# Kernel optimization log

Measured on AMD Instinct MI355X. Metric: run time of the kernel, lower is better.

The kernel has to match this reference:

```python
import jax, jax.numpy as jnp
import numpy as np

WS = 49        # window size
NH = 8         # num heads


def setup_inputs() -> dict:
    key = jax.random.key(0)
    k1, k2, k3 = jax.random.split(key, 3)
    B, N, C = 4, 50176, 512
    x = jax.random.normal(k1, (B, N, C), dtype=jnp.float32)
    w_qkv = jax.random.normal(k2, (3 * C, C), dtype=jnp.float32) * (C ** -0.5)
    b_qkv = jnp.zeros((3 * C,), dtype=jnp.float32)
    w_proj = jax.random.normal(k3, (C, C), dtype=jnp.float32) * (C ** -0.5)
    b_proj = jnp.zeros((C,), dtype=jnp.float32)
    return {"x": x, "w_qkv": w_qkv, "b_qkv": b_qkv, "w_proj": w_proj, "b_proj": b_proj}


def reference(x, w_qkv, b_qkv, w_proj, b_proj):
    B, N, C = x.shape
    w = N // WS
    hd = C // NH
    scale = hd ** -0.5
    # shuffle: 'b (ws w) c -> (b w) ws c'  (outer factor is ws -> strided windows)
    xw = x.reshape(B, WS, w, C).transpose(0, 2, 1, 3).reshape(B * w, WS, C)
    qkv = xw @ w_qkv.T + b_qkv                       # [(B w), WS, 3C]
    qkv = qkv.reshape(B * w, WS, 3, NH, hd)
    q = qkv[:, :, 0].transpose(0, 2, 1, 3) * scale   # [(B w), NH, WS, hd]
    k = qkv[:, :, 1].transpose(0, 2, 1, 3)
    v = qkv[:, :, 2].transpose(0, 2, 1, 3)
    attn = jax.nn.softmax(jnp.einsum('bhqd,bhkd->bhqk', q, k), axis=-1)
    out = jnp.einsum('bhqk,bhkd->bhqd', attn, v)     # [(B w), NH, WS, hd]
    out = out.transpose(0, 2, 1, 3).reshape(B * w, WS, C)
    out = out @ w_proj.T + b_proj
    # unshuffle: '(b w) ws c -> b (ws w) c'
    out = out.reshape(B, w, WS, C).transpose(0, 2, 1, 3).reshape(B, N, C)
    return out
```

## Files before the change

kernel.cpp:

```cpp
#include <hip/hip_runtime.h>
#include <cstdint>
#include <cstddef>


typedef __bf16 bf16x8 __attribute__((ext_vector_type(8)));
typedef __bf16 bf16x4 __attribute__((ext_vector_type(4)));
typedef float  f32x4  __attribute__((ext_vector_type(4)));

#define MFMA_BF16(a, b, c) __builtin_amdgcn_mfma_f32_16x16x32_bf16((a), (b), (c), 0, 0, 0)

static __device__ __forceinline__ int swzi(int row, int col) {
  return col ^ ((row & 7) << 3);
}
static __device__ __forceinline__ int gswz(int row, int col) {
  return col ^ (((row >> 1) & 3) << 3);
}

typedef __attribute__((address_space(1))) const void gconst_t;
typedef __attribute__((address_space(3))) void lds_t;
static __device__ __forceinline__ void gload16(const void* g, void* l) {
  __builtin_amdgcn_global_load_lds((gconst_t*)g, (lds_t*)l, 16, 0, 0);
}

__global__ void prep_weights(const float* __restrict__ wqkv,
                             const float* __restrict__ bqkv,
                             const float* __restrict__ wproj,
                             __bf16* __restrict__ wqkv_bf,
                             __bf16* __restrict__ wproj_bf,
                             float* __restrict__ bq_s) {
  const int stride = gridDim.x * blockDim.x;
  const int t0 = blockIdx.x * blockDim.x + threadIdx.x;
  for (int i = t0; i < 1536 * 512; i += stride) {
    float v = wqkv[i];
    if (i < 512 * 512) v *= 0.125f;
    wqkv_bf[i] = (__bf16)v;
  }
  for (int i = t0; i < 512 * 512; i += stride) wproj_bf[i] = (__bf16)wproj[i];
  for (int i = t0; i < 1536; i += stride)      bq_s[i] = (i < 512 ? 0.125f : 1.0f) * bqkv[i];
}

__global__ void prep_x(const float* __restrict__ x, __bf16* __restrict__ xb) {
  const size_t total  = (size_t)200704 * 512 / 8;
  const size_t stride = (size_t)gridDim.x * blockDim.x;
  for (size_t i = (size_t)blockIdx.x * blockDim.x + threadIdx.x; i < total; i += stride) {
    const float4 a = *(const float4*)(x + i * 8);
    const float4 b = *(const float4*)(x + i * 8 + 4);
    bf16x8 t;
    t[0] = (__bf16)a.x; t[1] = (__bf16)a.y; t[2] = (__bf16)a.z; t[3] = (__bf16)a.w;
    t[4] = (__bf16)b.x; t[5] = (__bf16)b.y; t[6] = (__bf16)b.z; t[7] = (__bf16)b.w;
    *(bf16x8*)(xb + i * 8) = t;
  }
}

template<bool OUT_F32>
__launch_bounds__(256)
__global__ void gemm_bt(const __bf16* __restrict__ Ab,
                        const __bf16* __restrict__ Bw,
                        const float* __restrict__ bias,
                        void* __restrict__ Cv,
                        int Mtiles, int Ntiles) {
  __shared__ __align__(16) __bf16 sA[2][128 * 32];
  __shared__ __align__(16) __bf16 sB[2][128 * 32];

  const int tid  = threadIdx.x;
  const int lane = tid & 63;
  const int l15  = lane & 15;
  const int kg   = ((lane >> 4) & 3) * 8;
  const int r4   = ((lane >> 4) & 3) * 4;
  const int wv   = tid >> 6, wm = wv >> 1, wn = wv & 1;

  const int nwg = Mtiles * Ntiles;
  const int cpx = nwg >> 3;
  const int wg  = (blockIdx.x & 7) * cpx + (blockIdx.x >> 3);
  const int mt  = wg / Ntiles;
  const int nt  = wg % Ntiles;
  const size_t m0 = (size_t)mt * 128;
  const int    n0 = nt * 128;

  const int srow  = tid >> 2;
  const int scol8 = ((tid & 3) * 8) ^ (((tid >> 3) & 3) << 3);

  f32x4 acc[4][4];
  const f32x4 zf = {0.f, 0.f, 0.f, 0.f};
#pragma unroll
  for (int i = 0; i < 4; ++i)
#pragma unroll
    for (int j = 0; j < 4; ++j) acc[i][j] = zf;

#pragma unroll
  for (int j = 0; j < 2; ++j) {
    gload16(Bw + ((size_t)(n0 + j * 64 + srow)) * 512 + scol8,
            &sB[0][0] + (size_t)tid * 8 + j * 2048);
    gload16(Ab + (m0 + j * 64 + srow) * 512 + scol8,
            &sA[0][0] + (size_t)tid * 8 + j * 2048);
  }
  __syncthreads();

  int buf = 0;
  for (int kt = 0; kt < 16; ++kt) {
    const int k1 = (kt + 1) * 32;
    if (kt < 15) {
#pragma unroll
      for (int j = 0; j < 2; ++j) {
        gload16(Bw + ((size_t)(n0 + j * 64 + srow)) * 512 + k1 + scol8,
                &sB[buf ^ 1][0] + (size_t)tid * 8 + j * 2048);
        gload16(Ab + (m0 + j * 64 + srow) * 512 + k1 + scol8,
                &sA[buf ^ 1][0] + (size_t)tid * 8 + j * 2048);
      }
    }
    bf16x8 af[4], bfr[4];
#pragma unroll
    for (int m = 0; m < 4; ++m) {
      const int row = wm * 64 + m * 16 + l15;
      af[m] = *(const bf16x8*)&sA[buf][row * 32 + gswz(row, kg)];
    }
#pragma unroll
    for (int n = 0; n < 4; ++n) {
      const int row = wn * 64 + n * 16 + l15;
      bfr[n] = *(const bf16x8*)&sB[buf][row * 32 + gswz(row, kg)];
    }
#pragma unroll
    for (int m = 0; m < 4; ++m)
#pragma unroll
      for (int n = 0; n < 4; ++n)
        acc[m][n] = MFMA_BF16(af[m], bfr[n], acc[m][n]);

    __syncthreads();
    buf ^= 1;
  }

  const int Nld = Ntiles * 128;
#pragma unroll
  for (int n = 0; n < 4; ++n) {
    const int col = n0 + wn * 64 + n * 16 + l15;
    const float bb = bias[col];
#pragma unroll
    for (int m = 0; m < 4; ++m) {
#pragma unroll
      for (int r = 0; r < 4; ++r) {
        const size_t row = m0 + wm * 64 + m * 16 + r4 + r;
        const float v = acc[m][n][r] + bb;
        if (OUT_F32) ((float*)Cv)[row * (size_t)Nld + col] = v;
        else         ((__bf16*)Cv)[row * (size_t)Nld + col] = (__bf16)v;
      }
    }
  }
}

__launch_bounds__(512)
__global__ void attn_win(const __bf16* __restrict__ qkv, __bf16* __restrict__ O) {
  __shared__ __align__(16) __bf16 vT[8 * 64 * 64];
  __shared__ __align__(16) __bf16 sP[8][16 * 64];

  const int tid  = threadIdx.x;
  const int lane = tid & 63;
  const int h    = tid >> 6;
  const int l15  = lane & 15;
  const int kg   = ((lane >> 4) & 3) * 8;
  const int r4   = ((lane >> 4) & 3) * 4;

  const int blk = blockIdx.x;
  const int b   = blk >> 10;
  const int wi  = blk & 1023;
  const size_t tokbase = (size_t)b * 50176 + wi;

  const int MOFF[4] = {0, 16, 32, 33};
  const float NEG_INF = -__builtin_inff();

  bf16x8 aq[4][2], bk[4][2];
#pragma unroll
  for (int mt = 0; mt < 4; ++mt) {
    const size_t tok = tokbase + (size_t)(MOFF[mt] + l15) * 1024;
#pragma unroll
    for (int ks = 0; ks < 2; ++ks) {
      aq[mt][ks] = *(const bf16x8*)(qkv + tok * 1536 +       h * 64 + ks * 32 + kg);
      bk[mt][ks] = *(const bf16x8*)(qkv + tok * 1536 + 512 + h * 64 + ks * 32 + kg);
    }
  }

  for (int i = tid; i < 8 * 64 * 16; i += 512) {
    const int k = 48 + (i & 15);
    if (k != 48) {
      const int n  = (i >> 4) & 63;
      const int hh = i >> 10;
      vT[hh * 4096 + n * 64 + (k ^ ((n & 7) << 3))] = (__bf16)0.0f;
    }
  }
  for (int i = tid; i < 49 * 64; i += 512) {
    const int s  = i >> 6;
    const int c8 = (i & 63) * 8;
    bf16x8 v8 = *(const bf16x8*)(qkv + (tokbase + (size_t)s * 1024) * 1536 + 1024 + c8);
    const int hh = c8 >> 6;
#pragma unroll
    for (int j = 0; j < 8; ++j) {
      const int n = (c8 & 63) + j;
      vT[hh * 4096 + n * 64 + (s ^ ((n & 7) << 3))] = v8[j];
    }
  }
  __syncthreads();

  bf16x8 bv[4][2];
#pragma unroll
  for (int ntv = 0; ntv < 4; ++ntv) {
    const int n = ntv * 16 + l15;
#pragma unroll
    for (int ks = 0; ks < 2; ++ks)
      bv[ntv][ks] = *(const bf16x8*)&vT[h * 4096 + n * 64 + ((ks * 32 + kg) ^ ((n & 7) << 3))];
  }

  f32x4 accS[4][4];
  const f32x4 zf = {0.f, 0.f, 0.f, 0.f};
#pragma unroll
  for (int m = 0; m < 4; ++m)
#pragma unroll
    for (int n = 0; n < 4; ++n) accS[m][n] = zf;
#pragma unroll
  for (int ks = 0; ks < 2; ++ks)
#pragma unroll
    for (int m = 0; m < 4; ++m)
#pragma unroll
      for (int n = 0; n < 4; ++n)
        accS[m][n] = MFMA_BF16(aq[m][ks], bk[n][ks], accS[m][n]);

#pragma unroll
  for (int mt = 0; mt < 4; ++mt) {
#pragma unroll
    for (int r = 0; r < 4; ++r) {
      const int prow = r4 + r;
      const float sv0 = accS[mt][0][r];
      const float sv1 = accS[mt][1][r];
      const float sv2 = accS[mt][2][r];
      const float sv3 = (l15 == 15) ? accS[mt][3][r] : NEG_INF;
      float mx = fmaxf(fmaxf(sv0, sv1), fmaxf(sv2, sv3));
      mx = fmaxf(mx, __shfl_xor(mx, 1));
      mx = fmaxf(mx, __shfl_xor(mx, 2));
      mx = fmaxf(mx, __shfl_xor(mx, 4));
      mx = fmaxf(mx, __shfl_xor(mx, 8));
      const float e0 = __expf(sv0 - mx);
      const float e1 = __expf(sv1 - mx);
      const float e2 = __expf(sv2 - mx);
      const float e3 = __expf(sv3 - mx);
      float sum = e0 + e1 + e2 + e3;
      sum += __shfl_xor(sum, 1);
      sum += __shfl_xor(sum, 2);
      sum += __shfl_xor(sum, 4);
      sum += __shfl_xor(sum, 8);
      const float inv = 1.0f / sum;
      sP[h][prow * 64 + swzi(prow, 0  + l15)] = (__bf16)(e0 * inv);
      sP[h][prow * 64 + swzi(prow, 16 + l15)] = (__bf16)(e1 * inv);
      sP[h][prow * 64 + swzi(prow, 32 + l15)] = (__bf16)(e2 * inv);
      if (l15 == 15) sP[h][prow * 64 + swzi(prow, 48)] = (__bf16)(e3 * inv);
      if (l15 < 15)  sP[h][prow * 64 + swzi(prow, 49 + l15)] = (__bf16)0.0f;
    }
    bf16x8 ap[2];
#pragma unroll
    for (int ks = 0; ks < 2; ++ks)
      ap[ks] = *(const bf16x8*)&sP[h][l15 * 64 + swzi(l15, ks * 32 + kg)];
    f32x4 accO[4];
#pragma unroll
    for (int n = 0; n < 4; ++n) accO[n] = zf;
#pragma unroll
    for (int ks = 0; ks < 2; ++ks)
#pragma unroll
      for (int n = 0; n < 4; ++n)
        accO[n] = MFMA_BF16(ap[ks], bv[n][ks], accO[n]);
#pragma unroll
    for (int n = 0; n < 4; ++n) {
#pragma unroll
      for (int r = 0; r < 4; ++r) {
        const int row = MOFF[mt] + r4 + r;
        O[(tokbase + (size_t)row * 1024) * 512 + h * 64 + n * 16 + l15] =
            (__bf16)accO[n][r];
      }
    }
  }
}

__launch_bounds__(256, 2)
__global__ void swin_attn_fused(const float* __restrict__ x,
                                const __bf16* __restrict__ wqkv_bf,
                                const float* __restrict__ bq_s,
                                const __bf16* __restrict__ wproj_bf,
                                const float* __restrict__ bproj,
                                float* __restrict__ out) {
  __shared__ __align__(16) __bf16 s_xw[49 * 512];
  __shared__ __align__(16) __bf16 s_q [49 * 64];
  __shared__ __align__(16) __bf16 s_k [49 * 64];
  __shared__ __align__(16) __bf16 s_vT[64 * 64];
  __shared__ __align__(16) __bf16 s_p [49 * 64];

  const int tid  = threadIdx.x;
  const int lane = tid & 63;
  const int wv   = tid >> 6;
  const int l15  = lane & 15;
  const int kg   = (lane >> 4) * 8;
  const int r4   = (lane >> 4) * 4;
  const int blk = blockIdx.x;
  const int b   = blk >> 10;
  const int wi  = blk & 1023;
  const int MOFF[4] = {0, 16, 32, 33};
  const float NEG_INF = -__builtin_inff();

  for (int i = tid; i < 64 * 64; i += 256) s_vT[i] = (__bf16)0.0f;
  const float* xwin = x + ((size_t)b * 50176 + (size_t)wi) * 512;
  for (int idx = tid; idx < 49 * 128; idx += 256) {
    const int row = idx >> 7;
    const int c4  = (idx & 127) * 4;
    const float4 v = *(const float4*)(xwin + (size_t)row * (1024 * 512) + c4);
    bf16x4 t;
    t.x = (__bf16)v.x; t.y = (__bf16)v.y; t.z = (__bf16)v.z; t.w = (__bf16)v.w;
    *(bf16x4*)&s_xw[row * 512 + swzi(row, c4)] = t;
  }
  f32x4 accF[4][8];
  const f32x4 zf = {0.f, 0.f, 0.f, 0.f};
#pragma unroll
  for (int m = 0; m < 4; ++m)
#pragma unroll
    for (int n = 0; n < 8; ++n) accF[m][n] = zf;
  __syncthreads();

  for (int h = 0; h < 8; ++h) {
    f32x4 accA[4][3];
#pragma unroll
    for (int m = 0; m < 4; ++m)
#pragma unroll
      for (int n = 0; n < 3; ++n) accA[m][n] = zf;
    const __bf16* pB[3];
    float biasv[3];
#pragma unroll
    for (int nt = 0; nt < 3; ++nt) {
      const int c  = wv * 48 + nt * 16 + l15;
      const int wr = (c < 64) ? (h * 64 + c)
                   : (c < 128) ? (512 + h * 64 + (c - 64))
                               : (1024 + h * 64 + (c - 128));
      pB[nt]    = wqkv_bf + (size_t)wr * 512 + kg;
      biasv[nt] = bq_s[wr];
    }
#pragma unroll
    for (int ks = 0; ks < 16; ++ks) {
      bf16x8 a[4], bb[3];
#pragma unroll
      for (int mt = 0; mt < 4; ++mt) {
        const int row = MOFF[mt] + l15;
        a[mt] = *(const bf16x8*)&s_xw[row * 512 + swzi(row, ks * 32 + kg)];
      }
#pragma unroll
      for (int nt = 0; nt < 3; ++nt) bb[nt] = *(const bf16x8*)(pB[nt] + ks * 32);
#pragma unroll
      for (int mt = 0; mt < 4; ++mt)
#pragma unroll
        for (int nt = 0; nt < 3; ++nt)
          accA[mt][nt] = MFMA_BF16(a[mt], bb[nt], accA[mt][nt]);
    }
#pragma unroll
    for (int nt = 0; nt < 3; ++nt) {
      const int c = wv * 48 + nt * 16 + l15;
#pragma unroll
      for (int mt = 0; mt < 4; ++mt) {
#pragma unroll
        for (int r = 0; r < 4; ++r) {
          const int row = MOFF[mt] + r4 + r;
          const __bf16 bvv = (__bf16)(accA[mt][nt][r] + biasv[nt]);
          if (c < 64)       s_q[row * 64 + swzi(row, c)] = bvv;
          else if (c < 128) s_k[row * 64 + swzi(row, c - 64)] = bvv;
          else {
            const int vr = c - 128;
            s_vT[vr * 64 + swzi(vr, row)] = bvv;
          }
        }
      }
    }
    __syncthreads();

    const int R = MOFF[wv];
    bf16x8 aq[2], bkf[4][2];
#pragma unroll
    for (int ks2 = 0; ks2 < 2; ++ks2) {
      const int row = R + l15;
      aq[ks2] = *(const bf16x8*)&s_q[row * 64 + swzi(row, ks2 * 32 + kg)];
    }
#pragma unroll
    for (int nt = 0; nt < 4; ++nt) {
      const int row = MOFF[nt] + l15;
#pragma unroll
      for (int ks2 = 0; ks2 < 2; ++ks2)
        bkf[nt][ks2] = *(const bf16x8*)&s_k[row * 64 + swzi(row, ks2 * 32 + kg)];
    }
    f32x4 accS[4];
#pragma unroll
    for (int n = 0; n < 4; ++n) accS[n] = zf;
#pragma unroll
    for (int ks2 = 0; ks2 < 2; ++ks2)
#pragma unroll
      for (int nt = 0; nt < 4; ++nt)
        accS[nt] = MFMA_BF16(aq[ks2], bkf[nt][ks2], accS[nt]);
#pragma unroll
    for (int r = 0; r < 4; ++r) {
      const int row = R + r4 + r;
      const float sv0 = accS[0][r];
      const float sv1 = accS[1][r];
      const float sv2 = accS[2][r];
      const float sv3 = (l15 == 15) ? accS[3][r] : NEG_INF;
      float m = fmaxf(fmaxf(sv0, sv1), fmaxf(sv2, sv3));
      m = fmaxf(m, __shfl_xor(m, 1));
      m = fmaxf(m, __shfl_xor(m, 2));
      m = fmaxf(m, __shfl_xor(m, 4));
      m = fmaxf(m, __shfl_xor(m, 8));
      const float e0 = __expf(sv0 - m);
      const float e1 = __expf(sv1 - m);
      const float e2 = __expf(sv2 - m);
      const float e3 = __expf(sv3 - m);
      float s = e0 + e1 + e2 + e3;
      s += __shfl_xor(s, 1);
      s += __shfl_xor(s, 2);
      s += __shfl_xor(s, 4);
      s += __shfl_xor(s, 8);
      const float inv = 1.0f / s;
      s_p[row * 64 + swzi(row, 0  + l15)] = (__bf16)(e0 * inv);
      s_p[row * 64 + swzi(row, 16 + l15)] = (__bf16)(e1 * inv);
      s_p[row * 64 + swzi(row, 32 + l15)] = (__bf16)(e2 * inv);
      if (l15 == 15) s_p[row * 64 + swzi(row, 48)] = (__bf16)(e3 * inv);
      if (l15 < 15)  s_p[row * 64 + swzi(row, 49 + l15)] = (__bf16)0.0f;
    }
    bf16x8 ap[2], bv2[4][2];
#pragma unroll
    for (int ks2 = 0; ks2 < 2; ++ks2) {
      const int row = R + l15;
      ap[ks2] = *(const bf16x8*)&s_p[row * 64 + swzi(row, ks2 * 32 + kg)];
    }
#pragma unroll
    for (int nt = 0; nt < 4; ++nt) {
      const int row = nt * 16 + l15;
#pragma unroll
      for (int ks2 = 0; ks2 < 2; ++ks2)
        bv2[nt][ks2] = *(const bf16x8*)&s_vT[row * 64 + swzi(row, ks2 * 32 + kg)];
    }
    __syncthreads();
    f32x4 accO[4];
#pragma unroll
    for (int n = 0; n < 4; ++n) accO[n] = zf;
#pragma unroll
    for (int ks2 = 0; ks2 < 2; ++ks2)
#pragma unroll
      for (int nt = 0; nt < 4; ++nt)
        accO[nt] = MFMA_BF16(ap[ks2], bv2[nt][ks2], accO[nt]);
#pragma unroll
    for (int nt = 0; nt < 4; ++nt) {
#pragma unroll
      for (int r = 0; r < 4; ++r) {
        const int row = R + r4 + r;
        s_p[row * 64 + swzi(row, nt * 16 + l15)] = (__bf16)accO[nt][r];
      }
    }
    __syncthreads();
#pragma unroll
    for (int ks2 = 0; ks2 < 2; ++ks2) {
      bf16x8 ao[4], bw[8];
#pragma unroll
      for (int mt = 0; mt < 4; ++mt) {
        const int row = MOFF[mt] + l15;
        ao[mt] = *(const bf16x8*)&s_p[row * 64 + swzi(row, ks2 * 32 + kg)];
      }
#pragma unroll
      for (int nt = 0; nt < 8; ++nt) {
        const int cc = wv * 128 + nt * 16 + l15;
        bw[nt] = *(const bf16x8*)(wproj_bf + (size_t)cc * 512 + h * 64 + ks2 * 32 + kg);
      }
#pragma unroll
      for (int mt = 0; mt < 4; ++mt)
#pragma unroll
        for (int nt = 0; nt < 8; ++nt)
          accF[mt][nt] = MFMA_BF16(ao[mt], bw[nt], accF[mt][nt]);
    }
  }
#pragma unroll
  for (int nt = 0; nt < 8; ++nt) {
    const int cc = wv * 128 + nt * 16 + l15;
    const float bp = bproj[cc];
#pragma unroll
    for (int mt = 0; mt < 4; ++mt) {
#pragma unroll
      for (int r = 0; r < 4; ++r) {
        const int row = MOFF[mt] + r4 + r;
        if (mt < 3 || (r4 + r) == 15) {
          out[((size_t)b * 50176 + (size_t)row * 1024 + (size_t)wi) * 512 + cc] =
              accF[mt][nt][r] + bp;
        }
      }
    }
  }
}

extern "C" void kernel_launch(void* const* d_in, const int* in_sizes, int n_in,
                              void* d_out, int out_size, void* d_ws, size_t ws_size,
                              hipStream_t stream) {
  const float* x      = (const float*)d_in[0];
  const float* w_qkv  = (const float*)d_in[1];
  const float* b_qkv  = (const float*)d_in[2];
  const float* w_proj = (const float*)d_in[3];
  const float* b_proj = (const float*)d_in[4];
  float* outp = (float*)d_out;

  const size_t QKV_E = (size_t)200704 * 1536;
  const size_t O_E   = (size_t)200704 * 512;
  const size_t NEED  = (QKV_E + O_E + 786432 + 262144) * 2 + 1536 * 4;

  if (ws_size >= NEED) {
    __bf16* qkv      = (__bf16*)d_ws;
    __bf16* Obuf     = qkv + QKV_E;
    __bf16* wqkv_bf  = Obuf + O_E;
    __bf16* wproj_bf = wqkv_bf + 786432;
    float*  bq_s     = (float*)(wproj_bf + 262144);

    prep_weights<<<512, 256, 0, stream>>>(w_qkv, b_qkv, w_proj, wqkv_bf, wproj_bf, bq_s);
    prep_x<<<2048, 256, 0, stream>>>(x, Obuf);
    gemm_bt<false><<<1568 * 12, 256, 0, stream>>>(Obuf, wqkv_bf, bq_s, qkv, 1568, 12);
    attn_win<<<4096, 512, 0, stream>>>(qkv, Obuf);
    gemm_bt<true ><<<1568 * 4,  256, 0, stream>>>(Obuf, wproj_bf, b_proj, outp, 1568, 4);
  } else {
    __bf16* wqkv_bf  = (__bf16*)d_ws;
    __bf16* wproj_bf = wqkv_bf + 1536 * 512;
    float*  bq_s     = (float*)(wproj_bf + 512 * 512);
    prep_weights<<<1024, 256, 0, stream>>>(w_qkv, b_qkv, w_proj, wqkv_bf, wproj_bf, bq_s);
    swin_attn_fused<<<4096, 256, 0, stream>>>(x, wqkv_bf, bq_s, wproj_bf, b_proj, outp);
  }
}
```

Measured before the change: 1.156 ms.

## Replace 128x128 GEMM with 256x256 tile, 512-thread kernel using raw barriers

Both projection GEMMs move from 128x128x32 tiles with 256 threads to 256x256x64 tiles with 512 threads and 8 waves. Each wave now computes a 128x64 sub-tile. The LDS staging uses an XOR chunk swizzle and double buffering with explicit vmcnt waits and raw s_barrier in place of __syncthreads, and MFMA priority is raised via s_setprio. The aim is more data reuse per byte loaded and less synchronisation overhead. In exchange, LDS use is 128KB per block, giving one block per CU, and register pressure is higher.

```diff
diff --git a/kernel.cpp b/kernel.cpp
--- a/kernel.cpp
+++ b/kernel.cpp
@@ -11,9 +11,6 @@
 
 static __device__ __forceinline__ int swzi(int row, int col) {
   return col ^ ((row & 7) << 3);
-}
-static __device__ __forceinline__ int gswz(int row, int col) {
-  return col ^ (((row >> 1) & 3) << 3);
 }
 
 typedef __attribute__((address_space(1))) const void gconst_t;
@@ -21,6 +18,9 @@
 static __device__ __forceinline__ void gload16(const void* g, void* l) {
   __builtin_amdgcn_global_load_lds((gconst_t*)g, (lds_t*)l, 16, 0, 0);
 }
+
+#define RAW_BAR()  asm volatile("s_barrier" ::: "memory")
+#define WAITV(N)   asm volatile("s_waitcnt vmcnt(" #N ")" ::: "memory")
 
 __global__ void prep_weights(const float* __restrict__ wqkv,
                              const float* __restrict__ bqkv,
@@ -53,92 +53,110 @@
 }
 
 template<bool OUT_F32>
-__launch_bounds__(256)
-__global__ void gemm_bt(const __bf16* __restrict__ Ab,
+__launch_bounds__(512, 1)
+__global__ void gemm256(const __bf16* __restrict__ Ab,
                         const __bf16* __restrict__ Bw,
                         const float* __restrict__ bias,
                         void* __restrict__ Cv,
                         int Mtiles, int Ntiles) {
-  __shared__ __align__(16) __bf16 sA[2][128 * 32];
-  __shared__ __align__(16) __bf16 sB[2][128 * 32];
+  __shared__ __align__(16) __bf16 sA[2][256 * 64];
+  __shared__ __align__(16) __bf16 sB[2][256 * 64];
 
   const int tid  = threadIdx.x;
   const int lane = tid & 63;
   const int l15  = lane & 15;
-  const int kg   = ((lane >> 4) & 3) * 8;
-  const int r4   = ((lane >> 4) & 3) * 4;
-  const int wv   = tid >> 6, wm = wv >> 1, wn = wv & 1;
+  const int kgc  = (lane >> 4) & 3;
+  const int r4   = kgc * 4;
+  const int wv   = tid >> 6;
+  const int wm   = wv >> 2, wn = wv & 3;
 
   const int nwg = Mtiles * Ntiles;
   const int cpx = nwg >> 3;
   const int wg  = (blockIdx.x & 7) * cpx + (blockIdx.x >> 3);
   const int mt  = wg / Ntiles;
   const int nt  = wg % Ntiles;
-  const size_t m0 = (size_t)mt * 128;
-  const int    n0 = nt * 128;
-
-  const int srow  = tid >> 2;
-  const int scol8 = ((tid & 3) * 8) ^ (((tid >> 3) & 3) << 3);
-
-  f32x4 acc[4][4];
+  const size_t m0 = (size_t)mt * 256;
+  const int    n0 = nt * 256;
+
+  const int srow   = tid >> 3;
+  const int schunk = (tid & 7) ^ (srow & 7);
+
+  f32x4 acc[8][4];
   const f32x4 zf = {0.f, 0.f, 0.f, 0.f};
 #pragma unroll
-  for (int i = 0; i < 4; ++i)
+  for (int i = 0; i < 8; ++i)
 #pragma unroll
     for (int j = 0; j < 4; ++j) acc[i][j] = zf;
 
-#pragma unroll
-  for (int j = 0; j < 2; ++j) {
-    gload16(Bw + ((size_t)(n0 + j * 64 + srow)) * 512 + scol8,
-            &sB[0][0] + (size_t)tid * 8 + j * 2048);
-    gload16(Ab + (m0 + j * 64 + srow) * 512 + scol8,
-            &sA[0][0] + (size_t)tid * 8 + j * 2048);
-  }
-  __syncthreads();
-
-  int buf = 0;
-  for (int kt = 0; kt < 16; ++kt) {
-    const int k1 = (kt + 1) * 32;
-    if (kt < 15) {
-#pragma unroll
-      for (int j = 0; j < 2; ++j) {
-        gload16(Bw + ((size_t)(n0 + j * 64 + srow)) * 512 + k1 + scol8,
-                &sB[buf ^ 1][0] + (size_t)tid * 8 + j * 2048);
-        gload16(Ab + (m0 + j * 64 + srow) * 512 + k1 + scol8,
-                &sA[buf ^ 1][0] + (size_t)tid * 8 + j * 2048);
-      }
-    }
-    bf16x8 af[4], bfr[4];
-#pragma unroll
-    for (int m = 0; m < 4; ++m) {
-      const int row = wm * 64 + m * 16 + l15;
-      af[m] = *(const bf16x8*)&sA[buf][row * 32 + gswz(row, kg)];
-    }
-#pragma unroll
-    for (int n = 0; n < 4; ++n) {
-      const int row = wn * 64 + n * 16 + l15;
-      bfr[n] = *(const bf16x8*)&sB[buf][row * 32 + gswz(row, kg)];
-    }
-#pragma unroll
-    for (int m = 0; m < 4; ++m)
-#pragma unroll
-      for (int n = 0; n < 4; ++n)
-        acc[m][n] = MFMA_BF16(af[m], bfr[n], acc[m][n]);
-
-    __syncthreads();
-    buf ^= 1;
-  }
-
-  const int Nld = Ntiles * 128;
+  auto STAGE = [&](int bufi, int kt) {
+    const size_t kof = (size_t)kt * 64 + schunk * 8;
+#pragma unroll
+    for (int j = 0; j < 4; ++j) {
+      gload16(Ab + (m0 + (size_t)(j * 64 + srow)) * 512 + kof,
+              &sA[bufi][0] + j * 4096 + tid * 8);
+      gload16(Bw + ((size_t)(n0 + j * 64 + srow)) * 512 + kof,
+              &sB[bufi][0] + j * 4096 + tid * 8);
+    }
+  };
+
+  auto COMPUTE = [&](int bufi) {
+#pragma unroll
+    for (int ks = 0; ks < 2; ++ks) {
+      bf16x8 bfrag[4];
+#pragma unroll
+      for (int n = 0; n < 4; ++n) {
+        const int r = wn * 64 + n * 16 + l15;
+        bfrag[n] = *(const bf16x8*)&sB[bufi][r * 64 + (((ks * 4 + kgc) ^ (r & 7)) * 8)];
+      }
+#pragma unroll
+      for (int mh = 0; mh < 2; ++mh) {
+        bf16x8 afrag[4];
+#pragma unroll
+        for (int m2 = 0; m2 < 4; ++m2) {
+          const int r = wm * 128 + mh * 64 + m2 * 16 + l15;
+          afrag[m2] = *(const bf16x8*)&sA[bufi][r * 64 + (((ks * 4 + kgc) ^ (r & 7)) * 8)];
+        }
+        __builtin_amdgcn_s_setprio(1);
+#pragma unroll
+        for (int m2 = 0; m2 < 4; ++m2)
+#pragma unroll
+          for (int n = 0; n < 4; ++n)
+            acc[mh * 4 + m2][n] = MFMA_BF16(afrag[m2], bfrag[n], acc[mh * 4 + m2][n]);
+        __builtin_amdgcn_s_setprio(0);
+      }
+    }
+  };
+
+  STAGE(0, 0);
+
+  for (int tt = 0; tt < 8; tt += 2) {
+    RAW_BAR();
+    STAGE(1, tt + 1);
+    WAITV(8);
+    RAW_BAR();
+    COMPUTE(0);
+
+    RAW_BAR();
+    if (tt < 6) {
+      STAGE(0, tt + 2);
+      WAITV(8);
+    } else {
+      WAITV(0);
+    }
+    RAW_BAR();
+    COMPUTE(1);
+  }
+
+  const int Nld = Ntiles * 256;
 #pragma unroll
   for (int n = 0; n < 4; ++n) {
     const int col = n0 + wn * 64 + n * 16 + l15;
     const float bb = bias[col];
 #pragma unroll
-    for (int m = 0; m < 4; ++m) {
+    for (int m = 0; m < 8; ++m) {
 #pragma unroll
       for (int r = 0; r < 4; ++r) {
-        const size_t row = m0 + wm * 64 + m * 16 + r4 + r;
+        const size_t row = m0 + wm * 128 + m * 16 + r4 + r;
         const float v = acc[m][n][r] + bb;
         if (OUT_F32) ((float*)Cv)[row * (size_t)Nld + col] = v;
         else         ((__bf16*)Cv)[row * (size_t)Nld + col] = (__bf16)v;
@@ -514,9 +532,9 @@
 
     prep_weights<<<512, 256, 0, stream>>>(w_qkv, b_qkv, w_proj, wqkv_bf, wproj_bf, bq_s);
     prep_x<<<2048, 256, 0, stream>>>(x, Obuf);
-    gemm_bt<false><<<1568 * 12, 256, 0, stream>>>(Obuf, wqkv_bf, bq_s, qkv, 1568, 12);
+    gemm256<false><<<784 * 6, 512, 0, stream>>>(Obuf, wqkv_bf, bq_s, qkv, 784, 6);
     attn_win<<<4096, 512, 0, stream>>>(qkv, Obuf);
-    gemm_bt<true ><<<1568 * 4,  256, 0, stream>>>(Obuf, wproj_bf, b_proj, outp, 1568, 4);
+    gemm256<true ><<<784 * 2, 512, 0, stream>>>(Obuf, wproj_bf, b_proj, outp, 784, 2);
   } else {
     __bf16* wqkv_bf  = (__bf16*)d_ws;
     __bf16* wproj_bf = wqkv_bf + 1536 * 512;
```

Result: no change. 1.138 ms (-1.6%).

## Gather x into window-major order so attention reads contiguous window rows

Applied to the files above, without the earlier changes.

The x-to-bf16 conversion now gathers tokens into window-major row order. The QKV buffer is therefore contiguous per window, and the attention kernel reads 49 consecutive rows instead of rows strided by 1024 tokens. The un-shuffle moves into the projection GEMM epilogue, which scatters each output row to its original token position. This aims to improve locality of the qkv/O accesses in attention, at the cost of a strided gather in prep_x and integer divisions per row in the epilogue.

```diff
diff --git a/kernel.cpp b/kernel.cpp
--- a/kernel.cpp
+++ b/kernel.cpp
@@ -20,6 +20,14 @@
 typedef __attribute__((address_space(3))) void lds_t;
 static __device__ __forceinline__ void gload16(const void* g, void* l) {
   __builtin_amdgcn_global_load_lds((gconst_t*)g, (lds_t*)l, 16, 0, 0);
+}
+
+static __device__ __forceinline__ int wm2tok(int m) {
+  const int b   = m / 50176;
+  const int rem = m - b * 50176;
+  const int wi  = rem / 49;
+  const int s   = rem - wi * 49;
+  return b * 50176 + s * 1024 + wi;
 }
 
 __global__ void prep_weights(const float* __restrict__ wqkv,
@@ -40,19 +48,22 @@
 }
 
 __global__ void prep_x(const float* __restrict__ x, __bf16* __restrict__ xb) {
-  const size_t total  = (size_t)200704 * 512 / 8;
+  const size_t total  = (size_t)200704 * 64;
   const size_t stride = (size_t)gridDim.x * blockDim.x;
   for (size_t i = (size_t)blockIdx.x * blockDim.x + threadIdx.x; i < total; i += stride) {
-    const float4 a = *(const float4*)(x + i * 8);
-    const float4 b = *(const float4*)(x + i * 8 + 4);
-    bf16x8 t;
-    t[0] = (__bf16)a.x; t[1] = (__bf16)a.y; t[2] = (__bf16)a.z; t[3] = (__bf16)a.w;
-    t[4] = (__bf16)b.x; t[5] = (__bf16)b.y; t[6] = (__bf16)b.z; t[7] = (__bf16)b.w;
-    *(bf16x8*)(xb + i * 8) = t;
-  }
-}
-
-template<bool OUT_F32>
+    const int m  = (int)(i >> 6);
+    const int c8 = ((int)i & 63) * 8;
+    const size_t t = (size_t)wm2tok(m);
+    const float4 a = *(const float4*)(x + t * 512 + c8);
+    const float4 b = *(const float4*)(x + t * 512 + c8 + 4);
+    bf16x8 v;
+    v[0] = (__bf16)a.x; v[1] = (__bf16)a.y; v[2] = (__bf16)a.z; v[3] = (__bf16)a.w;
+    v[4] = (__bf16)b.x; v[5] = (__bf16)b.y; v[6] = (__bf16)b.z; v[7] = (__bf16)b.w;
+    *(bf16x8*)(xb + i * 8) = v;
+  }
+}
+
+template<bool OUT_F32, bool PERM_OUT>
 __launch_bounds__(256)
 __global__ void gemm_bt(const __bf16* __restrict__ Ab,
                         const __bf16* __restrict__ Bw,
@@ -131,17 +142,17 @@
 
   const int Nld = Ntiles * 128;
 #pragma unroll
-  for (int n = 0; n < 4; ++n) {
-    const int col = n0 + wn * 64 + n * 16 + l15;
-    const float bb = bias[col];
-#pragma unroll
-    for (int m = 0; m < 4; ++m) {
-#pragma unroll
-      for (int r = 0; r < 4; ++r) {
-        const size_t row = m0 + wm * 64 + m * 16 + r4 + r;
-        const float v = acc[m][n][r] + bb;
-        if (OUT_F32) ((float*)Cv)[row * (size_t)Nld + col] = v;
-        else         ((__bf16*)Cv)[row * (size_t)Nld + col] = (__bf16)v;
+  for (int m = 0; m < 4; ++m) {
+#pragma unroll
+    for (int r = 0; r < 4; ++r) {
+      const int row = (int)m0 + wm * 64 + m * 16 + r4 + r;
+      const size_t orow = PERM_OUT ? (size_t)wm2tok(row) : (size_t)row;
+#pragma unroll
+      for (int n = 0; n < 4; ++n) {
+        const int col = n0 + wn * 64 + n * 16 + l15;
+        const float v = acc[m][n][r] + bias[col];
+        if (OUT_F32) ((float*)Cv)[orow * (size_t)Nld + col] = v;
+        else         ((__bf16*)Cv)[orow * (size_t)Nld + col] = (__bf16)v;
       }
     }
   }
@@ -159,10 +170,7 @@
   const int kg   = ((lane >> 4) & 3) * 8;
   const int r4   = ((lane >> 4) & 3) * 4;
 
-  const int blk = blockIdx.x;
-  const int b   = blk >> 10;
-  const int wi  = blk & 1023;
-  const size_t tokbase = (size_t)b * 50176 + wi;
+  const size_t wbase = (size_t)blockIdx.x * 49;
 
   const int MOFF[4] = {0, 16, 32, 33};
   const float NEG_INF = -__builtin_inff();
@@ -170,7 +178,7 @@
   bf16x8 aq[4][2], bk[4][2];
 #pragma unroll
   for (int mt = 0; mt < 4; ++mt) {
-    const size_t tok = tokbase + (size_t)(MOFF[mt] + l15) * 1024;
+    const size_t tok = wbase + (size_t)(MOFF[mt] + l15);
 #pragma unroll
     for (int ks = 0; ks < 2; ++ks) {
       aq[mt][ks] = *(const bf16x8*)(qkv + tok * 1536 +       h * 64 + ks * 32 + kg);
@@ -189,7 +197,7 @@
   for (int i = tid; i < 49 * 64; i += 512) {
     const int s  = i >> 6;
     const int c8 = (i & 63) * 8;
-    bf16x8 v8 = *(const bf16x8*)(qkv + (tokbase + (size_t)s * 1024) * 1536 + 1024 + c8);
+    bf16x8 v8 = *(const bf16x8*)(qkv + (wbase + s) * 1536 + 1024 + c8);
     const int hh = c8 >> 6;
 #pragma unroll
     for (int j = 0; j < 8; ++j) {
@@ -269,8 +277,7 @@
 #pragma unroll
       for (int r = 0; r < 4; ++r) {
         const int row = MOFF[mt] + r4 + r;
-        O[(tokbase + (size_t)row * 1024) * 512 + h * 64 + n * 16 + l15] =
-            (__bf16)accO[n][r];
+        O[(wbase + row) * 512 + h * 64 + n * 16 + l15] = (__bf16)accO[n][r];
       }
     }
   }
@@ -514,9 +521,9 @@
 
     prep_weights<<<512, 256, 0, stream>>>(w_qkv, b_qkv, w_proj, wqkv_bf, wproj_bf, bq_s);
     prep_x<<<2048, 256, 0, stream>>>(x, Obuf);
-    gemm_bt<false><<<1568 * 12, 256, 0, stream>>>(Obuf, wqkv_bf, bq_s, qkv, 1568, 12);
+    gemm_bt<false, false><<<1568 * 12, 256, 0, stream>>>(Obuf, wqkv_bf, bq_s, qkv, 1568, 12);
     attn_win<<<4096, 512, 0, stream>>>(qkv, Obuf);
-    gemm_bt<true ><<<1568 * 4,  256, 0, stream>>>(Obuf, wproj_bf, b_proj, outp, 1568, 4);
+    gemm_bt<true, true><<<1568 * 4, 256, 0, stream>>>(Obuf, wproj_bf, b_proj, outp, 1568, 4);
   } else {
     __bf16* wqkv_bf  = (__bf16*)d_ws;
     __bf16* wproj_bf = wqkv_bf + 1536 * 512;
```

New measurement: 1.163 ms. No clear change (+0.6%).
